# Kernel optimization log

Measured on AMD Instinct MI355X. Metric: run time of the kernel, lower is better.

Reference implementation:

```python
import jax, jax.numpy as jnp
import numpy as np

N = 50000        # nodes
E_RAND = 800000  # random edges (avg degree 16)
F_IN = 512       # num_features
H = 128          # h_dim * num_heads = 16 * 8
C = 40           # num_classes
NEG_SLOPE = 0.2  # GATv2 default


def _glorot(key, shape):
    lim = float(np.sqrt(6.0 / (shape[0] + shape[1])))
    return jax.random.uniform(key, shape, jnp.float32, -lim, lim)


def setup_inputs() -> dict:
    key = jax.random.key(0)
    ks = jax.random.split(key, 12)
    src = jax.random.randint(ks[0], (E_RAND,), 0, N)
    dst = jax.random.randint(ks[1], (E_RAND,), 0, N)
    loop = jnp.arange(N)  # self-loops (GATv2Conv add_self_loops=True)
    edge_index = jnp.stack([jnp.concatenate([src, loop]),
                            jnp.concatenate([dst, loop])]).astype(jnp.int32)
    x = jax.random.normal(ks[2], (N, F_IN), jnp.float32)
    return {
        "x": x,
        "edge_index": edge_index,
        "W1l": _glorot(ks[3], (F_IN, H)), "b1l": jnp.zeros((H,), jnp.float32),
        "W1r": _glorot(ks[4], (F_IN, H)), "b1r": jnp.zeros((H,), jnp.float32),
        "a1": _glorot(ks[5], (H, 1)).reshape(H),
        "bias1": jnp.zeros((H,), jnp.float32),
        "W2l": _glorot(ks[6], (H, C)), "b2l": jnp.zeros((C,), jnp.float32),
        "W2r": _glorot(ks[7], (H, C)), "b2r": jnp.zeros((C,), jnp.float32),
        "a2": _glorot(ks[8], (C, 1)).reshape(C),
        "bias2": jnp.zeros((C,), jnp.float32),
    }


def gatv2_layer(x, src, dst, Wl, bl, Wr, br, att, bias, n):
    # PyG GATv2Conv, heads=1: xl = lin_l(x) (source side), xr = lin_r(x) (target side)
    xl = x @ Wl + bl                                   # [N, C_out]
    xr = x @ Wr + br                                   # [N, C_out]
    # edge score e_ij = a^T LeakyReLU(xl[j] + xr[i])
    e = jax.nn.leaky_relu(xl[src] + xr[dst], negative_slope=NEG_SLOPE) @ att  # [E]
    # segment softmax over edges grouped by destination node
    m = jax.ops.segment_max(e, dst, num_segments=n)    # every node has a self-loop
    ex = jnp.exp(e - m[dst])
    den = jax.ops.segment_sum(ex, dst, num_segments=n)
    alpha = ex / den[dst]                              # [E]
    # weighted scatter-aggregate of source-transformed features
    out = jax.ops.segment_sum(alpha[:, None] * xl[src], dst, num_segments=n)
    return out + bias


def reference(x, edge_index, W1l, b1l, W1r, b1r, a1, bias1,
              W2l, b2l, W2r, b2r, a2, bias2):
    # eval mode: dropout(p=0.6) is identity
    src, dst = edge_index[0], edge_index[1]
    n = x.shape[0]
    h = gatv2_layer(x, src, dst, W1l, b1l, W1r, b1r, a1, bias1, n)
    h = jax.nn.elu(h)
    h = gatv2_layer(h, src, dst, W2l, b2l, W2r, b2r, a2, bias2, n)
    return (h, jax.nn.log_softmax(h, axis=1))
```

## Files before the change

### kernel.cpp

```cpp
#include <hip/hip_runtime.h>
#include <hip/hip_bf16.h>
#include <math.h>

#define FIN 512
#define H1 128
#define C2 40
#define C2P 64

typedef __attribute__((ext_vector_type(8))) short short8;
typedef __attribute__((ext_vector_type(4))) float f32x4;

__device__ __forceinline__ ushort f2bf(float f) {
    union { float f; unsigned u; } c; c.f = f;
    unsigned u = c.u;
    return (ushort)((u + 0x7fffu + ((u >> 16) & 1u)) >> 16);
}
__device__ __forceinline__ float bf2f_lo(unsigned u) { return __uint_as_float(u << 16); }
__device__ __forceinline__ float bf2f_hi(unsigned u) { return __uint_as_float(u & 0xffff0000u); }

__device__ __forceinline__ short bfc(float f) {
    __hip_bfloat16 h = __float2bfloat16(f);
    return *reinterpret_cast<short*>(&h);
}

__device__ __forceinline__ void gload_lds16(const void* g, void* l) {
    __builtin_amdgcn_global_load_lds(
        (const __attribute__((address_space(1))) void*)g,
        (__attribute__((address_space(3))) void*)l, 16, 0, 0);
}

__global__ void aux_k(const int* __restrict__ dst, int* __restrict__ cnt, int E, int EB,
                      const float* __restrict__ W1l, const float* __restrict__ W1r,
                      ushort* __restrict__ Wt2,
                      const float* __restrict__ W2l, const float* __restrict__ W2r,
                      ushort* __restrict__ Ws) {
    int b = blockIdx.x;
    int t = threadIdx.x;
    if (b < EB) {
        int e = b * 256 + t;
        if (e < E) atomicAdd(&cnt[dst[e] + 1], 1);
    } else if (b < EB + 512) {
        int idx = (b - EB) * 256 + t;
        int kc  = idx >> 11;
        int rem = idx & 2047;
        int col = rem >> 3;
        int j   = rem & 7;
        int k   = kc * 8 + j;
        float v = (col < H1) ? W1l[k * H1 + col] : W1r[k * H1 + (col - H1)];
        Wt2[idx] = f2bf(v);
    } else {
        int idx = (b - EB - 512) * 256 + t;
        if (idx < 80 * H1) {
            int col = idx >> 7;
            int k   = idx & 127;
            float v = (col < C2) ? W2l[k * C2 + col] : W2r[k * C2 + (col - C2)];
            Ws[idx] = f2bf(v);
        }
    }
}

__global__ __launch_bounds__(1024) void scan_k(int* __restrict__ arr, int ntot) {
    __shared__ int part[1024];
    int t = threadIdx.x;
    int chunk = (((ntot + 1023) / 1024) + 3) & ~3;
    int b = t * chunk;
    int s = 0;
    bool full = (b + chunk <= ntot);
    if (full) {
#pragma unroll 4
        for (int j = 0; j < chunk; j += 4) {
            int4 v = *reinterpret_cast<const int4*>(&arr[b + j]);
            s += v.x + v.y + v.z + v.w;
        }
    } else {
        for (int j = b; j < ntot; j++) s += arr[j];
    }
    part[t] = s;
    __syncthreads();
    for (int off = 1; off < 1024; off <<= 1) {
        int v = (t >= off) ? part[t - off] : 0;
        __syncthreads();
        part[t] += v;
        __syncthreads();
    }
    int run = (t == 0) ? 0 : part[t - 1];
    if (full) {
        for (int j = 0; j < chunk; j += 4) {
            int4 v = *reinterpret_cast<const int4*>(&arr[b + j]);
            int r0 = run + v.x, r1 = r0 + v.y, r2 = r1 + v.z, r3 = r2 + v.w;
            *reinterpret_cast<int4*>(&arr[b + j]) = make_int4(r0, r1, r2, r3);
            run = r3;
        }
    } else {
        for (int j = b; j < ntot; j++) { run += arr[j]; arr[j] = run; }
    }
}

__global__ void fill_k(const int* __restrict__ src, const int* __restrict__ dst,
                       const int* __restrict__ rowptr, int* __restrict__ fillp,
                       int* __restrict__ csr, int E) {
    int e = blockIdx.x * 256 + threadIdx.x;
    if (e < E) {
        int d = dst[e];
        int p = atomicAdd(&fillp[d], 1);
        csr[rowptr[d] + p] = src[e];
    }
}

__global__ __launch_bounds__(256, 3) void gemm1_k(
    const float* __restrict__ x, const ushort* __restrict__ Wt2,
    const float* __restrict__ bl, const float* __restrict__ br,
    ushort* __restrict__ xlb, float* __restrict__ xr, int n)
{
    __shared__ ushort As[64][72];
    __shared__ ushort Bs[8 * 256 * 8];

    const int tid  = threadIdx.x;
    const int w    = tid >> 6;
    const int lane = tid & 63;
    const int l15  = lane & 15;
    const int lhi  = lane >> 4;
    const int r0   = blockIdx.x * 64;

    f32x4 acc[4][4];
#pragma unroll
    for (int m = 0; m < 4; m++)
#pragma unroll
        for (int nn = 0; nn < 4; nn++) acc[m][nn] = (f32x4){0.f, 0.f, 0.f, 0.f};

    const int arow = tid >> 2;
    const int akq  = (tid & 3) * 16;
    const int arow_g = min(r0 + arow, n - 1);
    const float* aptr = x + (size_t)arow_g * FIN + akq;

    const char* bsrc = (const char*)Wt2 + (size_t)w * 8192 + (size_t)lane * 16;
    char*       bdst = (char*)Bs + (size_t)w * 8192 + (size_t)lane * 16;

    for (int kk = 0; kk < FIN; kk += 64) {
        const char* bs = bsrc + (size_t)(kk >> 3) * 4096;
#pragma unroll
        for (int i = 0; i < 8; i++)
            gload_lds16(bs + i * 1024, bdst + i * 1024);

        float4 v0 = *reinterpret_cast<const float4*>(aptr + kk);
        float4 v1 = *reinterpret_cast<const float4*>(aptr + kk + 4);
        float4 v2 = *reinterpret_cast<const float4*>(aptr + kk + 8);
        float4 v3 = *reinterpret_cast<const float4*>(aptr + kk + 12);
        short8 h0, h1;
        h0[0] = bfc(v0.x); h0[1] = bfc(v0.y); h0[2] = bfc(v0.z); h0[3] = bfc(v0.w);
        h0[4] = bfc(v1.x); h0[5] = bfc(v1.y); h0[6] = bfc(v1.z); h0[7] = bfc(v1.w);
        h1[0] = bfc(v2.x); h1[1] = bfc(v2.y); h1[2] = bfc(v2.z); h1[3] = bfc(v2.w);
        h1[4] = bfc(v3.x); h1[5] = bfc(v3.y); h1[6] = bfc(v3.z); h1[7] = bfc(v3.w);
        *reinterpret_cast<short8*>(&As[arow][akq])     = h0;
        *reinterpret_cast<short8*>(&As[arow][akq + 8]) = h1;

        __syncthreads();

#pragma unroll
        for (int ks = 0; ks < 2; ks++) {
            short8 af[4], bf4[4];
#pragma unroll
            for (int m = 0; m < 4; m++)
                af[m] = *reinterpret_cast<const short8*>(&As[m * 16 + l15][ks * 32 + lhi * 8]);
#pragma unroll
            for (int nn = 0; nn < 4; nn++)
                bf4[nn] = *reinterpret_cast<const short8*>(
                    &Bs[((ks * 4 + lhi) * 256 + w * 64 + nn * 16 + l15) * 8]);
#pragma unroll
            for (int m = 0; m < 4; m++)
#pragma unroll
                for (int nn = 0; nn < 4; nn++)
                    acc[m][nn] = __builtin_amdgcn_mfma_f32_16x16x32_bf16(af[m], bf4[nn], acc[m][nn], 0, 0, 0);
        }
        __syncthreads();
    }

#pragma unroll
    for (int nn = 0; nn < 4; nn++) {
        int col = w * 64 + nn * 16 + l15;
        bool left = (col < H1);
        float bias = left ? bl[col] : br[col - H1];
#pragma unroll
        for (int m = 0; m < 4; m++) {
#pragma unroll
            for (int r = 0; r < 4; r++) {
                int row = r0 + m * 16 + lhi * 4 + r;
                if (row < n) {
                    float v = acc[m][nn][r] + bias;
                    if (left) xlb[(size_t)row * H1 + col] = f2bf(v);
                    else      xr [(size_t)row * H1 + (col - H1)] = v;
                }
            }
        }
    }
}

__global__ __launch_bounds__(256) void edge1_k(
    const ushort* __restrict__ xlb, const float* xr,
    const int* __restrict__ rowptr, const int* __restrict__ csr,
    const float* __restrict__ att, const float* __restrict__ bias,
    float* h, int n)
{
    int wid  = threadIdx.x >> 6;
    int lane = threadIdx.x & 63;
    int grp  = lane >> 4;
    int gl   = lane & 15;
    int i = blockIdx.x * 4 + wid;
    if (i >= n) return;

    const float* xrp = &xr[(size_t)i * H1 + gl * 8];
    float4 xr0 = *reinterpret_cast<const float4*>(xrp);
    float4 xr1v = *reinterpret_cast<const float4*>(xrp + 4);
    float xrv[8] = {xr0.x, xr0.y, xr0.z, xr0.w, xr1v.x, xr1v.y, xr1v.z, xr1v.w};
    float4 a0 = *reinterpret_cast<const float4*>(&att[gl * 8]);
    float4 a1 = *reinterpret_cast<const float4*>(&att[gl * 8 + 4]);
    float av[8] = {a0.x, a0.y, a0.z, a0.w, a1.x, a1.y, a1.z, a1.w};

    int e0 = rowptr[i], e1 = rowptr[i + 1];

    float m = -INFINITY, den = 0.f;
    float acc[8];
#pragma unroll
    for (int f = 0; f < 8; f++) acc[f] = 0.f;

    int e = e0 + grp;
    uint4 u;
    if (e < e1) {
        int s = csr[e];
        u = *reinterpret_cast<const uint4*>(&xlb[(size_t)s * H1 + gl * 8]);
    }
    while (e < e1) {
        uint4 cu = u;
        int en = e + 4;
        if (en < e1) {
            int s2 = csr[en];
            u = *reinterpret_cast<const uint4*>(&xlb[(size_t)s2 * H1 + gl * 8]);
        }
        float xlv[8];
        xlv[0] = bf2f_lo(cu.x); xlv[1] = bf2f_hi(cu.x);
        xlv[2] = bf2f_lo(cu.y); xlv[3] = bf2f_hi(cu.y);
        xlv[4] = bf2f_lo(cu.z); xlv[5] = bf2f_hi(cu.z);
        xlv[6] = bf2f_lo(cu.w); xlv[7] = bf2f_hi(cu.w);
        float p = 0.f;
#pragma unroll
        for (int f = 0; f < 8; f++) {
            float t = xlv[f] + xrv[f];
            t = t > 0.f ? t : 0.2f * t;
            p += t * av[f];
        }
#pragma unroll
        for (int o = 8; o > 0; o >>= 1) p += __shfl_xor(p, o);
        float mn = fmaxf(m, p);
        float sc = __expf(m - mn);
        float wgt = __expf(p - mn);
        den = den * sc + wgt;
#pragma unroll
        for (int f = 0; f < 8; f++) acc[f] = acc[f] * sc + wgt * xlv[f];
        m = mn;
        e = en;
    }

    float mstar = m;
    mstar = fmaxf(mstar, __shfl_xor(mstar, 16));
    mstar = fmaxf(mstar, __shfl_xor(mstar, 32));
    float scale = __expf(m - mstar);
    den *= scale;
#pragma unroll
    for (int f = 0; f < 8; f++) acc[f] *= scale;
    den += __shfl_xor(den, 16); den += __shfl_xor(den, 32);
#pragma unroll
    for (int f = 0; f < 8; f++) {
        acc[f] += __shfl_xor(acc[f], 16);
        acc[f] += __shfl_xor(acc[f], 32);
    }

    if (grp == 0) {
        float inv = 1.f / den;
        float o[8];
#pragma unroll
        for (int f = 0; f < 8; f++) {
            float v = acc[f] * inv + bias[gl * 8 + f];
            o[f] = v > 0.f ? v : expm1f(v);
        }
        float* hp = &h[(size_t)i * H1 + gl * 8];
        *reinterpret_cast<float4*>(hp)     = make_float4(o[0], o[1], o[2], o[3]);
        *reinterpret_cast<float4*>(hp + 4) = make_float4(o[4], o[5], o[6], o[7]);
    }
}

__global__ __launch_bounds__(256) void gemm2_k(
    const float* __restrict__ h, const ushort* __restrict__ Ws,
    const float* __restrict__ bl, const float* __restrict__ br,
    ushort* __restrict__ xl2b, float* __restrict__ xr2, int n)
{
    __shared__ ushort WsL[80][136];

    const int tid = threadIdx.x;
    const int w    = tid >> 6;
    const int lane = tid & 63;
    const int l15  = lane & 15;
    const int lhi  = lane >> 4;
    const int r0 = blockIdx.x * 64;

#pragma unroll
    for (int q = 0; q < 5; q++) {
        int c = tid + q * 256;
        int col = c >> 4;
        int k0  = (c & 15) * 8;
        *reinterpret_cast<short8*>(&WsL[col][k0]) =
            *reinterpret_cast<const short8*>(&Ws[col * H1 + k0]);
    }
    __syncthreads();

    const int arow = min(r0 + w * 16 + l15, n - 1);
    const float* ap = &h[(size_t)arow * H1 + lhi * 8];

    f32x4 acc[5];
#pragma unroll
    for (int nt = 0; nt < 5; nt++) acc[nt] = (f32x4){0.f, 0.f, 0.f, 0.f};

#pragma unroll
    for (int kc = 0; kc < 4; kc++) {
        float4 v0 = *reinterpret_cast<const float4*>(ap + kc * 32);
        float4 v1 = *reinterpret_cast<const float4*>(ap + kc * 32 + 4);
        short8 af;
        af[0] = bfc(v0.x); af[1] = bfc(v0.y);
        af[2] = bfc(v0.z); af[3] = bfc(v0.w);
        af[4] = bfc(v1.x); af[5] = bfc(v1.y);
        af[6] = bfc(v1.z); af[7] = bfc(v1.w);
#pragma unroll
        for (int nt = 0; nt < 5; nt++) {
            short8 bf = *reinterpret_cast<const short8*>(&WsL[nt * 16 + l15][kc * 32 + lhi * 8]);
            acc[nt] = __builtin_amdgcn_mfma_f32_16x16x32_bf16(af, bf, acc[nt], 0, 0, 0);
        }
    }

#pragma unroll
    for (int nt = 0; nt < 5; nt++) {
        int col = nt * 16 + l15;
        float bias = (col < C2) ? bl[col] : br[col - C2];
#pragma unroll
        for (int r = 0; r < 4; r++) {
            int row = r0 + w * 16 + lhi * 4 + r;
            if (row < n) {
                float v = acc[nt][r] + bias;
                if (col < C2) xl2b[(size_t)row * C2P + col] = f2bf(v);
                else          xr2 [(size_t)row * C2  + (col - C2)] = v;
            }
        }
    }
    {
        int row = r0 + w * 16 + l15;
        int part = lhi;
        if (part < 3 && row < n) {
            uint4 z = make_uint4(0u, 0u, 0u, 0u);
            *reinterpret_cast<uint4*>(&xl2b[(size_t)row * C2P + C2 + part * 8]) = z;
        }
    }
}

__global__ __launch_bounds__(256) void edge2_k(
    const ushort* __restrict__ xl2b, const float* __restrict__ xr2,
    const int* __restrict__ rowptr, const int* __restrict__ csr,
    const float* __restrict__ att, const float* __restrict__ bias,
    float* __restrict__ out, int n)
{
    int wid  = threadIdx.x >> 6;
    int lane = threadIdx.x & 63;
    int grp  = lane >> 3;
    int gl   = lane & 7;
    int i = blockIdx.x * 4 + wid;
    if (i >= n) return;

    float xrv[8], av[8];
#pragma unroll
    for (int f = 0; f < 8; f++) {
        int idx = gl * 8 + f;
        bool real = idx < C2;
        xrv[f] = real ? xr2[(size_t)i * C2 + idx] : 0.f;
        av[f]  = real ? att[idx] : 0.f;
    }

    int e0 = rowptr[i], e1 = rowptr[i + 1];

    float m = -INFINITY, den = 0.f;
    float acc[8];
#pragma unroll
    for (int f = 0; f < 8; f++) acc[f] = 0.f;

    int e = e0 + grp;
    uint4 u;
    if (e < e1) {
        int s = csr[e];
        u = *reinterpret_cast<const uint4*>(&xl2b[(size_t)s * C2P + gl * 8]);
    }
    while (e < e1) {
        uint4 cu = u;
        int en = e + 8;
        if (en < e1) {
            int s2 = csr[en];
            u = *reinterpret_cast<const uint4*>(&xl2b[(size_t)s2 * C2P + gl * 8]);
        }
        float xlv[8];
        xlv[0] = bf2f_lo(cu.x); xlv[1] = bf2f_hi(cu.x);
        xlv[2] = bf2f_lo(cu.y); xlv[3] = bf2f_hi(cu.y);
        xlv[4] = bf2f_lo(cu.z); xlv[5] = bf2f_hi(cu.z);
        xlv[6] = bf2f_lo(cu.w); xlv[7] = bf2f_hi(cu.w);
        float p = 0.f;
#pragma unroll
        for (int f = 0; f < 8; f++) {
            float t = xlv[f] + xrv[f];
            t = t > 0.f ? t : 0.2f * t;
            p += t * av[f];
        }
#pragma unroll
        for (int o = 4; o > 0; o >>= 1) p += __shfl_xor(p, o);
        float mn = fmaxf(m, p);
        float sc = __expf(m - mn);
        float wgt = __expf(p - mn);
        den = den * sc + wgt;
#pragma unroll
        for (int f = 0; f < 8; f++) acc[f] = acc[f] * sc + wgt * xlv[f];
        m = mn;
        e = en;
    }

    float mstar = m;
    mstar = fmaxf(mstar, __shfl_xor(mstar, 8));
    mstar = fmaxf(mstar, __shfl_xor(mstar, 16));
    mstar = fmaxf(mstar, __shfl_xor(mstar, 32));
    float scale = __expf(m - mstar);
    den *= scale;
#pragma unroll
    for (int f = 0; f < 8; f++) acc[f] *= scale;
    den += __shfl_xor(den, 8); den += __shfl_xor(den, 16); den += __shfl_xor(den, 32);
#pragma unroll
    for (int f = 0; f < 8; f++) {
        acc[f] += __shfl_xor(acc[f], 8);
        acc[f] += __shfl_xor(acc[f], 16);
        acc[f] += __shfl_xor(acc[f], 32);
    }

    float inv = 1.f / den;
    bool real_lane = gl < 5;
    float o[8];
#pragma unroll
    for (int f = 0; f < 8; f++) {
        int idx = gl * 8 + f;
        o[f] = acc[f] * inv + (idx < C2 ? bias[idx] : 0.f);
    }

    float mv = -INFINITY;
    if (real_lane) {
#pragma unroll
        for (int f = 0; f < 8; f++) mv = fmaxf(mv, o[f]);
    }
    mv = fmaxf(mv, __shfl_xor(mv, 1));
    mv = fmaxf(mv, __shfl_xor(mv, 2));
    mv = fmaxf(mv, __shfl_xor(mv, 4));
    float se = 0.f;
    if (real_lane) {
#pragma unroll
        for (int f = 0; f < 8; f++) se += __expf(o[f] - mv);
    }
    se += __shfl_xor(se, 1); se += __shfl_xor(se, 2); se += __shfl_xor(se, 4);
    float lse = mv + logf(se);

    if (grp == 0 && real_lane) {
        float* op = &out[(size_t)i * C2 + gl * 8];
        *reinterpret_cast<float4*>(op)     = make_float4(o[0], o[1], o[2], o[3]);
        *reinterpret_cast<float4*>(op + 4) = make_float4(o[4], o[5], o[6], o[7]);
        float* lp = &out[(size_t)n * C2 + (size_t)i * C2 + gl * 8];
        *reinterpret_cast<float4*>(lp)     = make_float4(o[0] - lse, o[1] - lse, o[2] - lse, o[3] - lse);
        *reinterpret_cast<float4*>(lp + 4) = make_float4(o[4] - lse, o[5] - lse, o[6] - lse, o[7] - lse);
    }
}

extern "C" void kernel_launch(void* const* d_in, const int* in_sizes, int n_in,
                              void* d_out, int out_size, void* d_ws, size_t ws_size,
                              hipStream_t stream) {
    const float* x    = (const float*)d_in[0];
    const int*   ei   = (const int*)  d_in[1];
    const float* W1l  = (const float*)d_in[2];
    const float* b1l  = (const float*)d_in[3];
    const float* W1r  = (const float*)d_in[4];
    const float* b1r  = (const float*)d_in[5];
    const float* a1   = (const float*)d_in[6];
    const float* bias1= (const float*)d_in[7];
    const float* W2l  = (const float*)d_in[8];
    const float* b2l  = (const float*)d_in[9];
    const float* W2r  = (const float*)d_in[10];
    const float* b2r  = (const float*)d_in[11];
    const float* a2   = (const float*)d_in[12];
    const float* bias2= (const float*)d_in[13];

    const int N = in_sizes[0] / FIN;
    const int E = in_sizes[1] / 2;
    const int* src = ei;
    const int* dst = ei + E;

    float*  xr1 = (float*)d_ws;
    float*  xr2 = xr1 + (size_t)N * H1;
    ushort* xlb = (ushort*)(xr2 + (size_t)N * C2);
    ushort* xl2b = xlb;
    ushort* Wt2 = xlb + (size_t)N * H1;
    ushort* Ws2 = Wt2 + 131072;
    int* rowptr = (int*)(Ws2 + 10240);
    int* fillp  = rowptr + (N + 1);
    int* csr    = fillp + N;

    const int EB = (E + 255) / 256;

    hipMemsetAsync(rowptr, 0, sizeof(int) * (size_t)(2 * N + 1), stream);
    aux_k<<<EB + 552, 256, 0, stream>>>(dst, rowptr, E, EB, W1l, W1r, Wt2, W2l, W2r, Ws2);
    scan_k<<<1, 1024, 0, stream>>>(rowptr, N + 1);
    fill_k<<<EB, 256, 0, stream>>>(src, dst, rowptr, fillp, csr, E);

    gemm1_k<<<(N + 63) / 64, 256, 0, stream>>>(x, Wt2, b1l, b1r, xlb, xr1, N);
    edge1_k<<<(N + 3) / 4, 256, 0, stream>>>(xlb, xr1, rowptr, csr, a1, bias1, xr1, N);
    gemm2_k<<<(N + 63) / 64, 256, 0, stream>>>(xr1, Ws2, b2l, b2r, xl2b, xr2, N);
    edge2_k<<<(N + 3) / 4, 256, 0, stream>>>(xl2b, xr2, rowptr, csr, a2, bias2, (float*)d_out, N);
}
```

Baseline: 292.5 us.

## Store xr and hidden activations in bf16 and split scan into multi-block passes

Replaces the single-block 1024-thread prefix scan over row counts with a three-kernel reduce/scan-totals/scan-apply scheme across many blocks. Also stores the layer-1 target projection xr and the ELU output h as bf16 instead of fp32. This halves their write and read traffic in gemm1, edge1 and gemm2 and removes the fp32-to-bf16 conversion in gemm2. The cost is two extra kernel launches and lower precision for xr in the attention score computation.

```diff
diff --git a/kernel.cpp b/kernel.cpp
--- a/kernel.cpp
+++ b/kernel.cpp
@@ -59,41 +59,50 @@
     }
 }
 
-__global__ __launch_bounds__(1024) void scan_k(int* __restrict__ arr, int ntot) {
-    __shared__ int part[1024];
+__global__ void scanA_k(const int* __restrict__ arr, int* __restrict__ tot, int ntot) {
+    __shared__ int red[256];
+    int b = blockIdx.x, t = threadIdx.x;
+    int idx = b * 256 + t;
+    int v = (idx < ntot) ? arr[idx] : 0;
+    red[t] = v;
+    __syncthreads();
+#pragma unroll
+    for (int o = 128; o > 0; o >>= 1) {
+        if (t < o) red[t] += red[t + o];
+        __syncthreads();
+    }
+    if (t == 0) tot[b] = red[0];
+}
+
+__global__ void scanB_k(int* __restrict__ tot, int nb) {
+    __shared__ int s[256];
     int t = threadIdx.x;
-    int chunk = (((ntot + 1023) / 1024) + 3) & ~3;
-    int b = t * chunk;
-    int s = 0;
-    bool full = (b + chunk <= ntot);
-    if (full) {
-#pragma unroll 4
-        for (int j = 0; j < chunk; j += 4) {
-            int4 v = *reinterpret_cast<const int4*>(&arr[b + j]);
-            s += v.x + v.y + v.z + v.w;
-        }
-    } else {
-        for (int j = b; j < ntot; j++) s += arr[j];
-    }
-    part[t] = s;
+    int v = (t < nb) ? tot[t] : 0;
+    s[t] = v;
     __syncthreads();
-    for (int off = 1; off < 1024; off <<= 1) {
-        int v = (t >= off) ? part[t - off] : 0;
-        __syncthreads();
-        part[t] += v;
-        __syncthreads();
-    }
-    int run = (t == 0) ? 0 : part[t - 1];
-    if (full) {
-        for (int j = 0; j < chunk; j += 4) {
-            int4 v = *reinterpret_cast<const int4*>(&arr[b + j]);
-            int r0 = run + v.x, r1 = r0 + v.y, r2 = r1 + v.z, r3 = r2 + v.w;
-            *reinterpret_cast<int4*>(&arr[b + j]) = make_int4(r0, r1, r2, r3);
-            run = r3;
-        }
-    } else {
-        for (int j = b; j < ntot; j++) { run += arr[j]; arr[j] = run; }
-    }
+    for (int o = 1; o < 256; o <<= 1) {
+        int x = (t >= o) ? s[t - o] : 0;
+        __syncthreads();
+        s[t] += x;
+        __syncthreads();
+    }
+    if (t < nb) tot[t] = s[t] - v;
+}
+
+__global__ void scanC_k(int* __restrict__ arr, const int* __restrict__ tot, int ntot) {
+    __shared__ int s[256];
+    int b = blockIdx.x, t = threadIdx.x;
+    int idx = b * 256 + t;
+    int v = (idx < ntot) ? arr[idx] : 0;
+    s[t] = v;
+    __syncthreads();
+    for (int o = 1; o < 256; o <<= 1) {
+        int x = (t >= o) ? s[t - o] : 0;
+        __syncthreads();
+        s[t] += x;
+        __syncthreads();
+    }
+    if (idx < ntot) arr[idx] = s[t] + tot[b];
 }
 
 __global__ void fill_k(const int* __restrict__ src, const int* __restrict__ dst,
@@ -110,7 +119,7 @@
 __global__ __launch_bounds__(256, 3) void gemm1_k(
     const float* __restrict__ x, const ushort* __restrict__ Wt2,
     const float* __restrict__ bl, const float* __restrict__ br,
-    ushort* __restrict__ xlb, float* __restrict__ xr, int n)
+    ushort* __restrict__ xlb, ushort* __restrict__ xrb, int n)
 {
     __shared__ ushort As[64][72];
     __shared__ ushort Bs[8 * 256 * 8];
@@ -180,26 +189,25 @@
         int col = w * 64 + nn * 16 + l15;
         bool left = (col < H1);
         float bias = left ? bl[col] : br[col - H1];
+        ushort* outp = left ? xlb : xrb;
+        int colw = left ? col : col - H1;
 #pragma unroll
         for (int m = 0; m < 4; m++) {
 #pragma unroll
             for (int r = 0; r < 4; r++) {
                 int row = r0 + m * 16 + lhi * 4 + r;
-                if (row < n) {
-                    float v = acc[m][nn][r] + bias;
-                    if (left) xlb[(size_t)row * H1 + col] = f2bf(v);
-                    else      xr [(size_t)row * H1 + (col - H1)] = v;
-                }
+                if (row < n)
+                    outp[(size_t)row * H1 + colw] = f2bf(acc[m][nn][r] + bias);
             }
         }
     }
 }
 
 __global__ __launch_bounds__(256) void edge1_k(
-    const ushort* __restrict__ xlb, const float* xr,
+    const ushort* __restrict__ xlb, const ushort* xrb,
     const int* __restrict__ rowptr, const int* __restrict__ csr,
     const float* __restrict__ att, const float* __restrict__ bias,
-    float* h, int n)
+    ushort* hb, int n)
 {
     int wid  = threadIdx.x >> 6;
     int lane = threadIdx.x & 63;
@@ -208,10 +216,12 @@
     int i = blockIdx.x * 4 + wid;
     if (i >= n) return;
 
-    const float* xrp = &xr[(size_t)i * H1 + gl * 8];
-    float4 xr0 = *reinterpret_cast<const float4*>(xrp);
-    float4 xr1v = *reinterpret_cast<const float4*>(xrp + 4);
-    float xrv[8] = {xr0.x, xr0.y, xr0.z, xr0.w, xr1v.x, xr1v.y, xr1v.z, xr1v.w};
+    uint4 xru = *reinterpret_cast<const uint4*>(&xrb[(size_t)i * H1 + gl * 8]);
+    float xrv[8];
+    xrv[0] = bf2f_lo(xru.x); xrv[1] = bf2f_hi(xru.x);
+    xrv[2] = bf2f_lo(xru.y); xrv[3] = bf2f_hi(xru.y);
+    xrv[4] = bf2f_lo(xru.z); xrv[5] = bf2f_hi(xru.z);
+    xrv[6] = bf2f_lo(xru.w); xrv[7] = bf2f_hi(xru.w);
     float4 a0 = *reinterpret_cast<const float4*>(&att[gl * 8]);
     float4 a1 = *reinterpret_cast<const float4*>(&att[gl * 8 + 4]);
     float av[8] = {a0.x, a0.y, a0.z, a0.w, a1.x, a1.y, a1.z, a1.w};
@@ -276,20 +286,19 @@
 
     if (grp == 0) {
         float inv = 1.f / den;
-        float o[8];
+        short8 hv;
 #pragma unroll
         for (int f = 0; f < 8; f++) {
             float v = acc[f] * inv + bias[gl * 8 + f];
-            o[f] = v > 0.f ? v : expm1f(v);
-        }
-        float* hp = &h[(size_t)i * H1 + gl * 8];
-        *reinterpret_cast<float4*>(hp)     = make_float4(o[0], o[1], o[2], o[3]);
-        *reinterpret_cast<float4*>(hp + 4) = make_float4(o[4], o[5], o[6], o[7]);
+            v = v > 0.f ? v : expm1f(v);
+            hv[f] = bfc(v);
+        }
+        *reinterpret_cast<short8*>(&hb[(size_t)i * H1 + gl * 8]) = hv;
     }
 }
 
 __global__ __launch_bounds__(256) void gemm2_k(
-    const float* __restrict__ h, const ushort* __restrict__ Ws,
+    const ushort* __restrict__ hb, const ushort* __restrict__ Ws,
     const float* __restrict__ bl, const float* __restrict__ br,
     ushort* __restrict__ xl2b, float* __restrict__ xr2, int n)
 {
@@ -313,7 +322,7 @@
     __syncthreads();
 
     const int arow = min(r0 + w * 16 + l15, n - 1);
-    const float* ap = &h[(size_t)arow * H1 + lhi * 8];
+    const ushort* ap = &hb[(size_t)arow * H1 + lhi * 8];
 
     f32x4 acc[5];
 #pragma unroll
@@ -321,13 +330,7 @@
 
 #pragma unroll
     for (int kc = 0; kc < 4; kc++) {
-        float4 v0 = *reinterpret_cast<const float4*>(ap + kc * 32);
-        float4 v1 = *reinterpret_cast<const float4*>(ap + kc * 32 + 4);
-        short8 af;
-        af[0] = bfc(v0.x); af[1] = bfc(v0.y);
-        af[2] = bfc(v0.z); af[3] = bfc(v0.w);
-        af[4] = bfc(v1.x); af[5] = bfc(v1.y);
-        af[6] = bfc(v1.z); af[7] = bfc(v1.w);
+        short8 af = *reinterpret_cast<const short8*>(ap + kc * 32);
 #pragma unroll
         for (int nt = 0; nt < 5; nt++) {
             short8 bf = *reinterpret_cast<const short8*>(&WsL[nt * 16 + l15][kc * 32 + lhi * 8]);
@@ -499,25 +502,29 @@
     const int* src = ei;
     const int* dst = ei + E;
 
-    float*  xr1 = (float*)d_ws;
-    float*  xr2 = xr1 + (size_t)N * H1;
-    ushort* xlb = (ushort*)(xr2 + (size_t)N * C2);
+    ushort* xrb  = (ushort*)d_ws;
+    ushort* xlb  = xrb + (size_t)N * H1;
     ushort* xl2b = xlb;
-    ushort* Wt2 = xlb + (size_t)N * H1;
-    ushort* Ws2 = Wt2 + 131072;
-    int* rowptr = (int*)(Ws2 + 10240);
-    int* fillp  = rowptr + (N + 1);
-    int* csr    = fillp + N;
+    float*  xr2  = (float*)(xlb + (size_t)N * H1);
+    ushort* Wt2  = (ushort*)(xr2 + (size_t)N * C2);
+    ushort* Ws2  = Wt2 + 131072;
+    int* rowptr  = (int*)(Ws2 + 10240);
+    int* fillp   = rowptr + (N + 1);
+    int* csr     = fillp + N;
+    int* tot     = csr + E;
 
     const int EB = (E + 255) / 256;
+    const int SB = (N + 1 + 255) / 256;
 
     hipMemsetAsync(rowptr, 0, sizeof(int) * (size_t)(2 * N + 1), stream);
     aux_k<<<EB + 552, 256, 0, stream>>>(dst, rowptr, E, EB, W1l, W1r, Wt2, W2l, W2r, Ws2);
-    scan_k<<<1, 1024, 0, stream>>>(rowptr, N + 1);
+    scanA_k<<<SB, 256, 0, stream>>>(rowptr, tot, N + 1);
+    scanB_k<<<1, 256, 0, stream>>>(tot, SB);
+    scanC_k<<<SB, 256, 0, stream>>>(rowptr, tot, N + 1);
     fill_k<<<EB, 256, 0, stream>>>(src, dst, rowptr, fillp, csr, E);
 
-    gemm1_k<<<(N + 63) / 64, 256, 0, stream>>>(x, Wt2, b1l, b1r, xlb, xr1, N);
-    edge1_k<<<(N + 3) / 4, 256, 0, stream>>>(xlb, xr1, rowptr, csr, a1, bias1, xr1, N);
-    gemm2_k<<<(N + 63) / 64, 256, 0, stream>>>(xr1, Ws2, b2l, b2r, xl2b, xr2, N);
+    gemm1_k<<<(N + 63) / 64, 256, 0, stream>>>(x, Wt2, b1l, b1r, xlb, xrb, N);
+    edge1_k<<<(N + 3) / 4, 256, 0, stream>>>(xlb, xrb, rowptr, csr, a1, bias1, xrb, N);
+    gemm2_k<<<(N + 63) / 64, 256, 0, stream>>>(xrb, Ws2, b2l, b2r, xl2b, xr2, N);
     edge2_k<<<(N + 3) / 4, 256, 0, stream>>>(xl2b, xr2, rowptr, csr, a2, bias2, (float*)d_out, N);
 }
```

New measurement: 269.8 us. -7.8%, faster.
